# Kernel optimization log

Measured on AMD Instinct MI355X. Metric: run time of the kernel, lower is better.

The kernel has to match this reference:

```python
import jax, jax.numpy as jnp
import numpy as np

DIM = 512
NUM_HEADS = 8
HEAD_DIM = DIM // NUM_HEADS        # 64
L_HEADS = 4                        # int(8 * 0.5)
H_HEADS = NUM_HEADS - L_HEADS      # 4
L_DIM = L_HEADS * HEAD_DIM         # 256
H_DIM = H_HEADS * HEAD_DIM         # 256
WS = 2                             # window_size
SCALE = HEAD_DIM ** -0.5
SEQ_LEN = 1024


def setup_inputs() -> dict:
    key = jax.random.key(0)
    ks = jax.random.split(key, 13)
    B, N, C = 16, 1024, DIM
    def w(k, shape, fan_in):
        return (jax.random.normal(k, shape, jnp.float32) / np.sqrt(fan_in)).astype(jnp.float32)
    return {
        "x": jax.random.normal(ks[0], (B, N, C), jnp.float32),
        "pos_emb": jax.random.normal(ks[1], (1, SEQ_LEN, C), jnp.float32) * 0.02,
        "l_q_w": w(ks[2], (C, L_DIM), C),
        "l_kv_w": w(ks[3], (C, 2 * L_DIM), C),
        "l_proj_w": w(ks[4], (L_DIM, L_DIM), L_DIM),
        "l_proj_b": jax.random.normal(ks[5], (L_DIM,), jnp.float32) * 0.01,
        "h_qkv_w": w(ks[6], (C, 3 * H_DIM), C),
        "h_proj_w": w(ks[7], (H_DIM, H_DIM), H_DIM),
        "h_proj_b": jax.random.normal(ks[8], (H_DIM,), jnp.float32) * 0.01,
        "in_proj_w": w(ks[9], (C, 3 * C), C),
        "in_proj_b": jax.random.normal(ks[10], (3 * C,), jnp.float32) * 0.01,
        "out_proj_w": w(ks[11], (C, C), C),
        "out_proj_b": jax.random.normal(ks[12], (C,), jnp.float32) * 0.01,
        "H": 32,
        "W": 32,
    }


def _hifi(xg, h_qkv_w, h_proj_w, h_proj_b, H, W):
    B, _, _, C = xg.shape
    hg, wg = H // WS, W // WS
    G, T = hg * wg, WS * WS
    # [B, hg, WS, wg, WS, C] -> [B, G, T, C] (window partition)
    xw = xg.reshape(B, hg, WS, wg, WS, C).transpose(0, 1, 3, 2, 4, 5).reshape(B, G, T, C)
    qkv = (xw @ h_qkv_w).reshape(B, G, T, 3, H_HEADS, HEAD_DIM)
    q = qkv[:, :, :, 0].transpose(0, 1, 3, 2, 4)  # [B,G,h,T,d]
    k = qkv[:, :, :, 1].transpose(0, 1, 3, 2, 4)
    v = qkv[:, :, :, 2].transpose(0, 1, 3, 2, 4)
    attn = jax.nn.softmax(jnp.einsum("bghtd,bghsd->bghts", q, k) * SCALE, axis=-1)
    o = jnp.einsum("bghts,bghsd->bghtd", attn, v)
    # window un-partition: [B,G,h,T,d] -> [B,H,W,h_dim]
    o = o.transpose(0, 1, 3, 2, 4).reshape(B, hg, wg, WS, WS, H_DIM)
    o = o.transpose(0, 1, 3, 2, 4, 5).reshape(B, H, W, H_DIM)
    return o @ h_proj_w + h_proj_b


def _lofi(xg, l_q_w, l_kv_w, l_proj_w, l_proj_b, H, W):
    B, _, _, C = xg.shape
    N = H * W
    q = (xg @ l_q_w).reshape(B, N, L_HEADS, HEAD_DIM)
    kv = (xg @ l_kv_w).reshape(B, N, 2, L_HEADS, HEAD_DIM)
    k, v = kv[:, :, 0], kv[:, :, 1]
    attn = jax.nn.softmax(jnp.einsum("bnhd,bmhd->bhnm", q, k) * SCALE, axis=-1)
    o = jnp.einsum("bhnm,bmhd->bnhd", attn, v).reshape(B, H, W, L_DIM)
    return o @ l_proj_w + l_proj_b


def _mha(y, in_proj_w, in_proj_b, out_proj_w, out_proj_b):
    B, N, C = y.shape
    qkv = y @ in_proj_w + in_proj_b
    q, k, v = jnp.split(qkv, 3, axis=-1)
    q = q.reshape(B, N, NUM_HEADS, HEAD_DIM)
    k = k.reshape(B, N, NUM_HEADS, HEAD_DIM)
    v = v.reshape(B, N, NUM_HEADS, HEAD_DIM)
    attn = jax.nn.softmax(jnp.einsum("bnhd,bmhd->bhnm", q, k) * SCALE, axis=-1)
    o = jnp.einsum("bhnm,bmhd->bnhd", attn, v).reshape(B, N, C)
    return o @ out_proj_w + out_proj_b


def reference(x, pos_emb, l_q_w, l_kv_w, l_proj_w, l_proj_b,
              h_qkv_w, h_proj_w, h_proj_b,
              in_proj_w, in_proj_b, out_proj_w, out_proj_b, H, W):
    B, N, C = x.shape
    x = x + pos_emb[:, :N, :]
    xg = x.reshape(B, H, W, C)
    hifi_out = _hifi(xg, h_qkv_w, h_proj_w, h_proj_b, H, W)
    lofi_out = _lofi(xg, l_q_w, l_kv_w, l_proj_w, l_proj_b, H, W)
    y = jnp.concatenate([hifi_out, lofi_out], axis=-1).reshape(B, N, C)
    return _mha(y, in_proj_w, in_proj_b, out_proj_w, out_proj_b)
```

## Files before the change

kernel.cpp:

```cpp
#include <hip/hip_runtime.h>

typedef unsigned short ushort_t;
typedef short bf16x8 __attribute__((ext_vector_type(8)));
typedef float f32x4 __attribute__((ext_vector_type(4)));
typedef float f32x16 __attribute__((ext_vector_type(16)));

#define DEV __device__ __forceinline__

DEV ushort_t f2bf(float f) {
  return (ushort_t)((__float_as_uint(f) + 0x8000u) >> 16);
}
DEV unsigned pk_bf16(float lo, float hi) {
  unsigned a = __float_as_uint(lo) + 0x8000u;
  unsigned b = __float_as_uint(hi) + 0x8000u;
  return __builtin_amdgcn_perm(b, a, 0x07060302);
}
DEV unsigned cvtpk_bf16(float lo, float hi) {
  unsigned r;
  asm("v_cvt_pk_bf16_f32 %0, %1, %2" : "=v"(r) : "v"(lo), "v"(hi));
  return r;
}
DEV float bf2f(ushort_t h) {
  union { unsigned int u; float f; } v; v.u = ((unsigned int)h) << 16;
  return v.f;
}
DEV f32x4 mfma16(bf16x8 a, bf16x8 b, f32x4 c) {
  return __builtin_amdgcn_mfma_f32_16x16x32_bf16(a, b, c, 0, 0, 0);
}
DEV f32x16 mfma32(bf16x8 a, bf16x8 b, f32x16 c) {
  return __builtin_amdgcn_mfma_f32_32x32x16_bf16(a, b, c, 0, 0, 0);
}
DEV void pl32swap(unsigned &a, unsigned &b) {
  asm("v_permlane32_swap_b32 %0, %1" : "+v"(a), "+v"(b));
}
typedef __attribute__((address_space(3))) void lds_void;
typedef const __attribute__((address_space(1))) void glb_void;
DEV void gl_lds16(const void* g, void* l) {
  __builtin_amdgcn_global_load_lds((glb_void*)g, (lds_void*)l, 16, 0, 0);
}

__global__ __launch_bounds__(256)
void gemm_bt(const ushort_t* __restrict__ A, int lda,
             const ushort_t* __restrict__ BT,
             const float* __restrict__ bias,
             ushort_t* __restrict__ Cb, float* __restrict__ Cf,
             int ldc, int coff, int K, float scv, int sc_lo, int sc_hi)
{
  __shared__ __align__(16) ushort_t As[128 * 32];
  __shared__ __align__(16) ushort_t Bs[128 * 32];
  const int tid  = threadIdx.x;
  const int wave = tid >> 6, lane = tid & 63;
  const int quad = lane >> 4, r16 = lane & 15;
  const int nwg = gridDim.x * gridDim.y;
  const int lin = blockIdx.x + gridDim.x * blockIdx.y;
  const int logical = (lin & 7) * (nwg >> 3) + (lin >> 3);
  const int nbn = gridDim.y;
  const int mb = logical / nbn, nb = logical - mb * nbn;
  const int m0 = mb * 128, n0 = nb * 128;
  const int wm = (wave >> 1) * 64, wn = (wave & 1) * 64;

  f32x4 acc[4][4];
#pragma unroll
  for (int i = 0; i < 4; ++i)
#pragma unroll
    for (int j = 0; j < 4; ++j) acc[i][j] = (f32x4){0.f, 0.f, 0.f, 0.f};

  auto stage = [&](int kc) {
#pragma unroll
    for (int p = 0; p < 4; ++p) {
      int wp = p * 4 + wave;
      int lc = ((wp & 7) << 6) + lane;
      int row = lc >> 2, e8 = (lc & 3) * 8;
      if (wp < 8) gl_lds16(&A[(size_t)(m0 + row) * lda + kc + e8], &As[lc * 8]);
      else        gl_lds16(&BT[(size_t)(n0 + row) * K  + kc + e8], &Bs[lc * 8]);
    }
  };

  stage(0);
  const int NI = K >> 5;
  for (int ki = 0; ki < NI; ++ki) {
    __syncthreads();
    bf16x8 af[4], bfr[4];
#pragma unroll
    for (int i = 0; i < 4; ++i) {
      af[i]  = *(const bf16x8*)&As[(wm + i * 16 + r16) * 32 + quad * 8];
      bfr[i] = *(const bf16x8*)&Bs[(wn + i * 16 + r16) * 32 + quad * 8];
    }
    __syncthreads();
    if (ki + 1 < NI) stage((ki + 1) << 5);
#pragma unroll
    for (int mi = 0; mi < 4; ++mi)
#pragma unroll
      for (int ni = 0; ni < 4; ++ni)
        acc[mi][ni] = mfma16(af[mi], bfr[ni], acc[mi][ni]);
  }

#pragma unroll
  for (int mi = 0; mi < 4; ++mi) {
#pragma unroll
    for (int ni = 0; ni < 4; ++ni) {
      int col = n0 + wn + ni * 16 + r16;
      float bv = bias ? bias[col] : 0.f;
      float s = (col >= sc_lo && col < sc_hi) ? scv : 1.0f;
#pragma unroll
      for (int r = 0; r < 4; ++r) {
        int row = m0 + wm + mi * 16 + quad * 4 + r;
        float v = (acc[mi][ni][r] + bv) * s;
        if (Cf) Cf[(size_t)row * ldc + coff + col] = v;
        else    Cb[(size_t)row * ldc + coff + col] = f2bf(v);
      }
    }
  }
}

__global__ __launch_bounds__(256)
void gemm_proj(const ushort_t* __restrict__ rB,
               const ushort_t* __restrict__ hT, const ushort_t* __restrict__ lT,
               const float* __restrict__ hb, const float* __restrict__ lb,
               ushort_t* __restrict__ y)
{
  __shared__ __align__(16) ushort_t As[128 * 32];
  __shared__ __align__(16) ushort_t Bs[128 * 32];
  const int tid  = threadIdx.x;
  const int wave = tid >> 6, lane = tid & 63;
  const int quad = lane >> 4, r16 = lane & 15;
  const int lin = blockIdx.x + 128 * blockIdx.y;
  const int logical = (lin & 7) * 64 + (lin >> 3);
  const int nidx = logical & 3, m0 = (logical >> 2) * 128;
  const int sel = nidx >> 1, n0 = (nidx & 1) * 128;
  const ushort_t* A  = rB + sel * 256;
  const ushort_t* BT = sel ? lT : hT;
  const float* bias  = sel ? lb : hb;
  const int coff = sel * 256;
  const int wm = (wave >> 1) * 64, wn = (wave & 1) * 64;

  f32x4 acc[4][4];
#pragma unroll
  for (int i = 0; i < 4; ++i)
#pragma unroll
    for (int j = 0; j < 4; ++j) acc[i][j] = (f32x4){0.f, 0.f, 0.f, 0.f};

  auto stage = [&](int kc) {
#pragma unroll
    for (int p = 0; p < 4; ++p) {
      int wp = p * 4 + wave;
      int lc = ((wp & 7) << 6) + lane;
      int row = lc >> 2, e8 = (lc & 3) * 8;
      if (wp < 8) gl_lds16(&A[(size_t)(m0 + row) * 512 + kc + e8], &As[lc * 8]);
      else        gl_lds16(&BT[(size_t)(n0 + row) * 256 + kc + e8], &Bs[lc * 8]);
    }
  };

  stage(0);
  for (int ki = 0; ki < 8; ++ki) {
    __syncthreads();
    bf16x8 af[4], bfr[4];
#pragma unroll
    for (int i = 0; i < 4; ++i) {
      af[i]  = *(const bf16x8*)&As[(wm + i * 16 + r16) * 32 + quad * 8];
      bfr[i] = *(const bf16x8*)&Bs[(wn + i * 16 + r16) * 32 + quad * 8];
    }
    __syncthreads();
    if (ki + 1 < 8) stage((ki + 1) << 5);
#pragma unroll
    for (int mi = 0; mi < 4; ++mi)
#pragma unroll
      for (int ni = 0; ni < 4; ++ni)
        acc[mi][ni] = mfma16(af[mi], bfr[ni], acc[mi][ni]);
  }

#pragma unroll
  for (int mi = 0; mi < 4; ++mi) {
#pragma unroll
    for (int ni = 0; ni < 4; ++ni) {
      int col = n0 + wn + ni * 16 + r16;
      float bv = bias[col];
#pragma unroll
      for (int r = 0; r < 4; ++r) {
        int row = m0 + wm + mi * 16 + quad * 4 + r;
        y[(size_t)row * 512 + coff + col] = f2bf(acc[mi][ni][r] + bv);
      }
    }
  }
}

template<int QG>
__global__ __launch_bounds__(256, 2)
void flash_attn9(const ushort_t* __restrict__ Q, int qs, int q_ch,
                 const ushort_t* __restrict__ Kg, int ks, int k_ch,
                 const ushort_t* __restrict__ vT,
                 ushort_t* __restrict__ O, int os, int o_ch,
                 int N)
{
  __shared__ __align__(16) ushort_t Ks[2][64 * 64];
  __shared__ __align__(16) ushort_t Vs[2][64 * 64];

  const int H = gridDim.y;
  const int tid = threadIdx.x, wave = tid >> 6, lane = tid & 63;
  const int c = lane & 31, hh = lane >> 5;

  const int nwg = gridDim.x * H * gridDim.z;
  const int lin = blockIdx.x + gridDim.x * (blockIdx.y + H * blockIdx.z);
  const int logical = (lin & 7) * (nwg >> 3) + (lin >> 3);
  const int QBS = 8 / QG;
  const int qb = logical & (QBS - 1);
  const int t8 = logical / QBS;
  const int b = (H == 8) ? (t8 >> 3) : (t8 >> 2);
  const int h = t8 - b * H;
  const int q0 = qb * (128 * QG) + wave * (32 * QG);

  bf16x8 qf[QG][4];
#pragma unroll
  for (int qg = 0; qg < QG; ++qg) {
    const ushort_t* qp =
        Q + ((size_t)b * N + q0 + qg * 32 + c) * qs + q_ch + h * 64 + hh * 8;
#pragma unroll
    for (int s = 0; s < 4; ++s) qf[qg][s] = *(const bf16x8*)&qp[s * 16];
  }
  const ushort_t* kbase = Kg + ((size_t)b * N) * ks + k_ch + h * 64;
  const ushort_t* vbase = vT + ((size_t)(b * H + h) * 64) * N;

  f32x16 oacc[QG][2];
#pragma unroll
  for (int qg = 0; qg < QG; ++qg)
#pragma unroll
    for (int i = 0; i < 16; ++i) { oacc[qg][0][i] = 0.f; oacc[qg][1][i] = 0.f; }
  float l_acc[QG];
#pragma unroll
  for (int qg = 0; qg < QG; ++qg) l_acc[qg] = 0.f;

  auto stage = [&](int s0, int buf) {
#pragma unroll
    for (int p = 0; p < 4; ++p) {
      int wp = p * 4 + wave;
      int lc = ((wp & 7) << 6) + lane;
      int row = lc >> 3, cc = lc & 7;
      int e8 = ((cc ^ (row & 7)) * 8);
      if (wp < 8) gl_lds16(kbase + (size_t)(s0 + row) * ks + e8, &Ks[buf][lc * 8]);
      else        gl_lds16(vbase + (size_t)row * N + s0 + e8,    &Vs[buf][lc * 8]);
    }
  };

  stage(0, 0);
  const int NT = N >> 6;
  for (int it = 0; it < NT; ++it) {
    const int cur = it & 1;
    __syncthreads();
    if (it + 1 < NT) stage((it + 1) << 6, cur ^ 1);

    bf16x8 Bf[QG][4];
#pragma unroll
    for (int kb = 0; kb < 2; ++kb) {
      const int krow = kb * 32 + c;
      const ushort_t* kr = &Ks[cur][krow * 64];
      bf16x8 kf[4];
#pragma unroll
      for (int s = 0; s < 4; ++s)
        kf[s] = *(const bf16x8*)&kr[(((s << 1) + hh) ^ (krow & 7)) * 8];

#pragma unroll
      for (int qg = 0; qg < QG; ++qg) {
        f32x16 z;
#pragma unroll
        for (int i = 0; i < 16; ++i) z[i] = 0.f;
#pragma unroll
        for (int s = 0; s < 4; ++s) z = mfma32(kf[s], qf[qg][s], z);
        float ts = 0.f;
        unsigned W[8];
#pragma unroll
        for (int t = 0; t < 8; ++t) {
          float p0 = __builtin_amdgcn_exp2f(z[2 * t]);
          float p1 = __builtin_amdgcn_exp2f(z[2 * t + 1]);
          ts += p0 + p1;
          W[t] = cvtpk_bf16(p0, p1);
        }
        l_acc[qg] += ts;
        union U8 { bf16x8 f; unsigned u[4]; } f0, f1;
        unsigned a0 = W[0], b0 = W[2]; pl32swap(a0, b0);
        unsigned a1 = W[1], b1 = W[3]; pl32swap(a1, b1);
        f0.u[0] = a0; f0.u[1] = a1; f0.u[2] = b0; f0.u[3] = b1;
        unsigned a2 = W[4], b2 = W[6]; pl32swap(a2, b2);
        unsigned a3 = W[5], b3 = W[7]; pl32swap(a3, b3);
        f1.u[0] = a2; f1.u[1] = a3; f1.u[2] = b2; f1.u[3] = b3;
        Bf[qg][kb * 2]     = f0.f;
        Bf[qg][kb * 2 + 1] = f1.f;
      }
    }

#pragma unroll
    for (int db = 0; db < 2; ++db) {
      const int vrow = db * 32 + c;
      const ushort_t* vr = &Vs[cur][vrow * 64];
      bf16x8 vf[4];
#pragma unroll
      for (int s = 0; s < 4; ++s)
        vf[s] = *(const bf16x8*)&vr[(((s << 1) + hh) ^ (vrow & 7)) * 8];
#pragma unroll
      for (int qg = 0; qg < QG; ++qg)
#pragma unroll
        for (int s = 0; s < 4; ++s)
          oacc[qg][db] = mfma32(vf[s], Bf[qg][s], oacc[qg][db]);
    }
  }

#pragma unroll
  for (int qg = 0; qg < QG; ++qg) {
    float l = l_acc[qg] + __shfl_xor(l_acc[qg], 32);
    float inv = 1.f / l;
    ushort_t* op = O + ((size_t)b * N + q0 + qg * 32 + c) * os + o_ch + h * 64;
#pragma unroll
    for (int db = 0; db < 2; ++db) {
#pragma unroll
      for (int g = 0; g < 4; ++g) {
        uint2 pkv;
        pkv.x = cvtpk_bf16(oacc[qg][db][4 * g + 0] * inv, oacc[qg][db][4 * g + 1] * inv);
        pkv.y = cvtpk_bf16(oacc[qg][db][4 * g + 2] * inv, oacc[qg][db][4 * g + 3] * inv);
        *(uint2*)&op[db * 32 + g * 8 + hh * 4] = pkv;
      }
    }
  }
}

__global__ __launch_bounds__(256)
void transpose_v(const ushort_t* __restrict__ in, int ld, int ch,
                 ushort_t* __restrict__ out, int N, int H)
{
  __shared__ __align__(16) ushort_t T[64][72];
  const int s0 = blockIdx.x * 64, h = blockIdx.y, b = blockIdx.z;
  const int tid = threadIdx.x;
#pragma unroll
  for (int p = 0; p < 2; ++p) {
    int c = p * 256 + tid;
    int sr = c >> 3, d0 = (c & 7) * 8;
    *(uint4*)&T[sr][d0] =
        *(const uint4*)&in[((size_t)b * N + s0 + sr) * ld + ch + h * 64 + d0];
  }
  __syncthreads();
  const int d = tid >> 2, sp = (tid & 3) * 16;
  union { uint4 v; ushort_t u[8]; } A, B;
#pragma unroll
  for (int j = 0; j < 8; ++j) { A.u[j] = T[sp + j][d]; B.u[j] = T[sp + 8 + j][d]; }
  ushort_t* op = out + ((size_t)(b * H + h) * 64 + d) * N + s0 + sp;
  *(uint4*)&op[0] = A.v;
  *(uint4*)&op[8] = B.v;
}

__global__ __launch_bounds__(256)
void hifi_win(const ushort_t* __restrict__ qkv, int ld, ushort_t* __restrict__ out)
{
  const int bg = blockIdx.x;
  const int b = bg >> 8, g = bg & 255;
  const int head = threadIdx.x >> 6, lane = threadIdx.x & 63;
  const int gh = g >> 4, gw = g & 15;

  int n[4];
  float q[4], k[4], v[4];
#pragma unroll
  for (int t = 0; t < 4; ++t) {
    n[t] = (gh * 2 + (t >> 1)) * 32 + gw * 2 + (t & 1);
    size_t base = ((size_t)b * 1024 + n[t]) * ld + head * 64 + lane;
    q[t] = bf2f(qkv[base]);
    k[t] = bf2f(qkv[base + 256]);
    v[t] = bf2f(qkv[base + 512]);
  }
  float sc[4][4];
#pragma unroll
  for (int t = 0; t < 4; ++t)
#pragma unroll
    for (int s = 0; s < 4; ++s) {
      float p = q[t] * k[s];
#pragma unroll
      for (int off = 32; off >= 1; off >>= 1) p += __shfl_xor(p, off);
      sc[t][s] = p * 0.125f;
    }
#pragma unroll
  for (int t = 0; t < 4; ++t) {
    float m = fmaxf(fmaxf(sc[t][0], sc[t][1]), fmaxf(sc[t][2], sc[t][3]));
    float p0 = __expf(sc[t][0] - m), p1 = __expf(sc[t][1] - m);
    float p2 = __expf(sc[t][2] - m), p3 = __expf(sc[t][3] - m);
    float sum = p0 + p1 + p2 + p3;
    float o = (p0 * v[0] + p1 * v[1] + p2 * v[2] + p3 * v[3]) / sum;
    out[((size_t)b * 1024 + n[t]) * 512 + head * 64 + lane] = f2bf(o);
  }
}

struct WEnt { const float* W; ushort_t* WT; int K; int N; };
struct WArgs { WEnt e[7]; };

__global__ __launch_bounds__(256)
void w_prep(WArgs a)
{
  WEnt w = a.e[blockIdx.z];
  if ((int)blockIdx.x >= (w.K >> 6) || (int)blockIdx.y >= (w.N >> 6)) return;
  __shared__ float T[64][65];
  const int k0 = blockIdx.x * 64, n0 = blockIdx.y * 64;
  const int tid = threadIdx.x;
#pragma unroll
  for (int p = 0; p < 4; ++p) {
    int c = p * 256 + tid;
    int kr = c >> 4, f4 = (c & 15) * 4;
    float4 v = *(const float4*)&w.W[(size_t)(k0 + kr) * w.N + n0 + f4];
    T[f4 + 0][kr] = v.x; T[f4 + 1][kr] = v.y;
    T[f4 + 2][kr] = v.z; T[f4 + 3][kr] = v.w;
  }
  __syncthreads();
  const int nl = tid >> 2, kp = (tid & 3) * 16;
  union { uint4 v; ushort_t u[8]; } A, B;
#pragma unroll
  for (int j = 0; j < 8; ++j) {
    A.u[j] = f2bf(T[nl][kp + j]);
    B.u[j] = f2bf(T[nl][kp + 8 + j]);
  }
  ushort_t* op = w.WT + (size_t)(n0 + nl) * w.K + k0 + kp;
  *(uint4*)&op[0] = A.v;
  *(uint4*)&op[8] = B.v;
}

__global__ void add_pos(const float* __restrict__ x, const float* __restrict__ pos,
                        ushort_t* __restrict__ xpe)
{
  int idx = blockIdx.x * 256 + threadIdx.x;
  int e = idx * 4;
  float4 xv = *(const float4*)&x[e];
  float4 pv = *(const float4*)&pos[e & (512 * 1024 - 1)];
  uint2 pk;
  pk.x = pk_bf16(xv.x + pv.x, xv.y + pv.y);
  pk.y = pk_bf16(xv.z + pv.z, xv.w + pv.w);
  *(uint2*)&xpe[e] = pk;
}

extern "C" void kernel_launch(void* const* d_in, const int* in_sizes, int n_in,
                              void* d_out, int out_size, void* d_ws, size_t ws_size,
                              hipStream_t stream)
{
  const float* x         = (const float*)d_in[0];
  const float* pos       = (const float*)d_in[1];
  const float* l_q_w     = (const float*)d_in[2];
  const float* l_kv_w    = (const float*)d_in[3];
  const float* l_proj_w  = (const float*)d_in[4];
  const float* l_proj_b  = (const float*)d_in[5];
  const float* h_qkv_w   = (const float*)d_in[6];
  const float* h_proj_w  = (const float*)d_in[7];
  const float* h_proj_b  = (const float*)d_in[8];
  const float* in_proj_w = (const float*)d_in[9];
  const float* in_proj_b = (const float*)d_in[10];
  const float* out_proj_w= (const float*)d_in[11];
  const float* out_proj_b= (const float*)d_in[12];
  float* out = (float*)d_out;

  const float QSCALE = 0.125f * 1.44269504f;

  char* ws = (char*)d_ws;
  ushort_t* xpe = (ushort_t*)(ws);
  ushort_t* y   = (ushort_t*)(ws + (size_t)16777216);
  ushort_t* F   = (ushort_t*)(ws + (size_t)33554432);
  ushort_t* rB  = (ushort_t*)(ws + (size_t)83886080);
  ushort_t* wb  = (ushort_t*)(ws + (size_t)100663296);

  ushort_t* F_T      = wb;
  ushort_t* h_projT  = wb + 786432;
  ushort_t* l_projT  = wb + 851968;
  ushort_t* in_projT = wb + 917504;
  ushort_t* out_projT= wb + 1703936;

  const int M = 16384;
  ushort_t* vT_lo = xpe;
  ushort_t* vT_m  = rB;

  WArgs wa;
  wa.e[0] = {h_qkv_w,   F_T,                 512, 768};
  wa.e[1] = {l_q_w,     F_T + 768 * 512,     512, 256};
  wa.e[2] = {l_kv_w,    F_T + 1024 * 512,    512, 512};
  wa.e[3] = {h_proj_w,  h_projT,             256, 256};
  wa.e[4] = {l_proj_w,  l_projT,             256, 256};
  wa.e[5] = {in_proj_w, in_projT,            512, 1536};
  wa.e[6] = {out_proj_w,out_projT,           512, 512};
  w_prep<<<dim3(8, 24, 7), dim3(256), 0, stream>>>(wa);

  add_pos<<<dim3(8192), dim3(256), 0, stream>>>(x, pos, xpe);

  gemm_bt<<<dim3(M / 128, 12), dim3(256), 0, stream>>>(
      xpe, 512, F_T, nullptr, F, nullptr, 1536, 0, 512, QSCALE, 768, 1024);
  hifi_win<<<dim3(4096), dim3(256), 0, stream>>>(F, 1536, rB);
  transpose_v<<<dim3(16, 4, 16), dim3(256), 0, stream>>>(
      F, 1536, 1280, vT_lo, 1024, 4);
  flash_attn9<1><<<dim3(8, 4, 16), dim3(256), 0, stream>>>(
      F, 1536, 768, F, 1536, 1024, vT_lo, rB, 512, 256, 1024);
  gemm_proj<<<dim3(128, 4), dim3(256), 0, stream>>>(
      rB, h_projT, l_projT, h_proj_b, l_proj_b, y);
  gemm_bt<<<dim3(M / 128, 12), dim3(256), 0, stream>>>(
      y, 512, in_projT, in_proj_b, F, nullptr, 1536, 0, 512, QSCALE, 0, 512);
  transpose_v<<<dim3(16, 8, 16), dim3(256), 0, stream>>>(
      F, 1536, 1024, vT_m, 1024, 8);
  flash_attn9<2><<<dim3(4, 8, 16), dim3(256), 0, stream>>>(
      F, 1536, 0, F, 1536, 512, vT_m, xpe, 512, 0, 1024);
  gemm_bt<<<dim3(M / 128, 4), dim3(256), 0, stream>>>(
      xpe, 512, out_projT, out_proj_b, nullptr, out, 512, 0, 512, 1.0f, 0, 0);
}
```

Measured before the change: 320.3 us.

## Fuse V transpose into projection GEMM epilogue via new gemm_vt kernel

Splits the V columns out of the QKV projection GEMMs into a new gemm_vt kernel that writes V directly in transposed (head, dim, seq) layout. This removes the two standalone transpose_v kernels and the round trip of V through global memory. The transposed epilogue writes strided 2-byte stores (one per element across a 1024 stride), which could coalesce poorly, and the vT_lo buffer moves to y to avoid aliasing with xpe, which is still being read.

```diff
diff --git a/kernel.cpp b/kernel.cpp
--- a/kernel.cpp
+++ b/kernel.cpp
@@ -108,6 +108,79 @@
         float v = (acc[mi][ni][r] + bv) * s;
         if (Cf) Cf[(size_t)row * ldc + coff + col] = v;
         else    Cb[(size_t)row * ldc + coff + col] = f2bf(v);
+      }
+    }
+  }
+}
+
+__global__ __launch_bounds__(256)
+void gemm_vt(const ushort_t* __restrict__ A, int lda,
+             const ushort_t* __restrict__ BT,
+             const float* __restrict__ bias,
+             ushort_t* __restrict__ vT, int H, int K)
+{
+  __shared__ __align__(16) ushort_t As[128 * 32];
+  __shared__ __align__(16) ushort_t Bs[128 * 32];
+  const int tid  = threadIdx.x;
+  const int wave = tid >> 6, lane = tid & 63;
+  const int quad = lane >> 4, r16 = lane & 15;
+  const int nwg = gridDim.x * gridDim.y;
+  const int lin = blockIdx.x + gridDim.x * blockIdx.y;
+  const int logical = (lin & 7) * (nwg >> 3) + (lin >> 3);
+  const int nbn = gridDim.y;
+  const int mb = logical / nbn, nb = logical - mb * nbn;
+  const int m0 = mb * 128, n0 = nb * 128;
+  const int wm = (wave >> 1) * 64, wn = (wave & 1) * 64;
+
+  f32x4 acc[4][4];
+#pragma unroll
+  for (int i = 0; i < 4; ++i)
+#pragma unroll
+    for (int j = 0; j < 4; ++j) acc[i][j] = (f32x4){0.f, 0.f, 0.f, 0.f};
+
+  auto stage = [&](int kc) {
+#pragma unroll
+    for (int p = 0; p < 4; ++p) {
+      int wp = p * 4 + wave;
+      int lc = ((wp & 7) << 6) + lane;
+      int row = lc >> 2, e8 = (lc & 3) * 8;
+      if (wp < 8) gl_lds16(&A[(size_t)(m0 + row) * lda + kc + e8], &As[lc * 8]);
+      else        gl_lds16(&BT[(size_t)(n0 + row) * K  + kc + e8], &Bs[lc * 8]);
+    }
+  };
+
+  stage(0);
+  const int NI = K >> 5;
+  for (int ki = 0; ki < NI; ++ki) {
+    __syncthreads();
+    bf16x8 af[4], bfr[4];
+#pragma unroll
+    for (int i = 0; i < 4; ++i) {
+      af[i]  = *(const bf16x8*)&As[(wm + i * 16 + r16) * 32 + quad * 8];
+      bfr[i] = *(const bf16x8*)&Bs[(wn + i * 16 + r16) * 32 + quad * 8];
+    }
+    __syncthreads();
+    if (ki + 1 < NI) stage((ki + 1) << 5);
+#pragma unroll
+    for (int mi = 0; mi < 4; ++mi)
+#pragma unroll
+      for (int ni = 0; ni < 4; ++ni)
+        acc[mi][ni] = mfma16(bfr[ni], af[mi], acc[mi][ni]);
+  }
+
+#pragma unroll
+  for (int mi = 0; mi < 4; ++mi) {
+    const int row = m0 + wm + mi * 16 + r16;
+    const int b = row >> 10, nl = row & 1023;
+    ushort_t* vb = vT + ((size_t)b * H * 64) * 1024 + nl;
+#pragma unroll
+    for (int ni = 0; ni < 4; ++ni) {
+      const int col = n0 + wn + ni * 16 + quad * 4;
+      float4 bv = bias ? *(const float4*)&bias[col]
+                       : make_float4(0.f, 0.f, 0.f, 0.f);
+#pragma unroll
+      for (int r = 0; r < 4; ++r) {
+        vb[(size_t)(col + r) * 1024] = f2bf(acc[mi][ni][r] + (&bv.x)[r]);
       }
     }
   }
@@ -322,30 +395,6 @@
 }
 
 __global__ __launch_bounds__(256)
-void transpose_v(const ushort_t* __restrict__ in, int ld, int ch,
-                 ushort_t* __restrict__ out, int N, int H)
-{
-  __shared__ __align__(16) ushort_t T[64][72];
-  const int s0 = blockIdx.x * 64, h = blockIdx.y, b = blockIdx.z;
-  const int tid = threadIdx.x;
-#pragma unroll
-  for (int p = 0; p < 2; ++p) {
-    int c = p * 256 + tid;
-    int sr = c >> 3, d0 = (c & 7) * 8;
-    *(uint4*)&T[sr][d0] =
-        *(const uint4*)&in[((size_t)b * N + s0 + sr) * ld + ch + h * 64 + d0];
-  }
-  __syncthreads();
-  const int d = tid >> 2, sp = (tid & 3) * 16;
-  union { uint4 v; ushort_t u[8]; } A, B;
-#pragma unroll
-  for (int j = 0; j < 8; ++j) { A.u[j] = T[sp + j][d]; B.u[j] = T[sp + 8 + j][d]; }
-  ushort_t* op = out + ((size_t)(b * H + h) * 64 + d) * N + s0 + sp;
-  *(uint4*)&op[0] = A.v;
-  *(uint4*)&op[8] = B.v;
-}
-
-__global__ __launch_bounds__(256)
 void hifi_win(const ushort_t* __restrict__ qkv, int ld, ushort_t* __restrict__ out)
 {
   const int bg = blockIdx.x;
@@ -464,7 +513,7 @@
   ushort_t* out_projT= wb + 1703936;
 
   const int M = 16384;
-  ushort_t* vT_lo = xpe;
+  ushort_t* vT_lo = y;
   ushort_t* vT_m  = rB;
 
   WArgs wa;
@@ -479,19 +528,19 @@
 
   add_pos<<<dim3(8192), dim3(256), 0, stream>>>(x, pos, xpe);
 
-  gemm_bt<<<dim3(M / 128, 12), dim3(256), 0, stream>>>(
+  gemm_bt<<<dim3(M / 128, 10), dim3(256), 0, stream>>>(
       xpe, 512, F_T, nullptr, F, nullptr, 1536, 0, 512, QSCALE, 768, 1024);
+  gemm_vt<<<dim3(M / 128, 2), dim3(256), 0, stream>>>(
+      xpe, 512, F_T + 1280 * 512, nullptr, vT_lo, 4, 512);
   hifi_win<<<dim3(4096), dim3(256), 0, stream>>>(F, 1536, rB);
-  transpose_v<<<dim3(16, 4, 16), dim3(256), 0, stream>>>(
-      F, 1536, 1280, vT_lo, 1024, 4);
   flash_attn9<1><<<dim3(8, 4, 16), dim3(256), 0, stream>>>(
       F, 1536, 768, F, 1536, 1024, vT_lo, rB, 512, 256, 1024);
   gemm_proj<<<dim3(128, 4), dim3(256), 0, stream>>>(
       rB, h_projT, l_projT, h_proj_b, l_proj_b, y);
-  gemm_bt<<<dim3(M / 128, 12), dim3(256), 0, stream>>>(
+  gemm_bt<<<dim3(M / 128, 8), dim3(256), 0, stream>>>(
       y, 512, in_projT, in_proj_b, F, nullptr, 1536, 0, 512, QSCALE, 0, 512);
-  transpose_v<<<dim3(16, 8, 16), dim3(256), 0, stream>>>(
-      F, 1536, 1024, vT_m, 1024, 8);
+  gemm_vt<<<dim3(M / 128, 4), dim3(256), 0, stream>>>(
+      y, 512, in_projT + 1024 * 512, in_proj_b + 1024, vT_m, 8, 512);
   flash_attn9<2><<<dim3(4, 8, 16), dim3(256), 0, stream>>>(
       F, 1536, 0, F, 1536, 512, vT_m, xpe, 512, 0, 1024);
   gemm_bt<<<dim3(M / 128, 4), dim3(256), 0, stream>>>(
```

After: 320.9 us. No clear change (+0.2%).
